# Optimization experiments

Measured on AMD Instinct MI355X. Metric: run time of the kernel, lower is better.

The kernel has to match this reference:

```python
import jax, jax.numpy as jnp
import numpy as np

N, S, E, H = 4, 4096, 1024, 16
D = E // H  # 64


def setup_inputs() -> dict:
    key = jax.random.key(0)
    ks = jax.random.split(key, 6)
    scale = 0.02
    x = jax.random.normal(ks[0], (N, S, E), dtype=jnp.float32)
    Wq = jax.random.normal(ks[1], (E, E), dtype=jnp.float32) * scale
    Wk = jax.random.normal(ks[2], (E, E), dtype=jnp.float32) * scale
    Wv = jax.random.normal(ks[3], (E, E), dtype=jnp.float32) * scale
    Wo = jax.random.normal(ks[4], (E, E), dtype=jnp.float32) * scale
    bo = jax.random.normal(ks[5], (E,), dtype=jnp.float32) * scale
    return {"x": x, "Wq": Wq, "Wk": Wk, "Wv": Wv, "Wo": Wo, "bo": bo}


def reference(x, Wq, Wk, Wv, Wo, bo):
    n, s, _ = x.shape
    # torch nn.Linear(bias=False): y = x @ W.T  (W stored as [out, in])
    q = (x @ Wq.T).reshape(n, s, H, D).transpose(0, 2, 1, 3)  # (N, H, S, D)
    k = (x @ Wk.T).reshape(n, s, H, D).transpose(0, 2, 1, 3)  # (N, H, S, D)
    v = (x @ Wv.T).reshape(n, s, H, D).transpose(0, 2, 1, 3)  # (N, H, S, D)
    # Faithful to source: einsum subscripts applied to the PERMUTED (N,H,S,D)
    # tensors, so label q->H, h->S. energy: (N, H, H, S)
    energy = jnp.einsum('nqhd,nkhd->nqkh', q, k)
    attention = jax.nn.softmax(energy / (D ** 0.5), axis=3)
    # 'nqkh,nvhd->nqhd': k and v are independently summed free indices
    out = jnp.einsum('nqkh,nvhd->nqhd', attention, v).reshape(n, s, E)  # (N,S,E)
    return out @ Wo.T + bo
```

## Files before the change

### kernel.cpp

```cpp
#include <hip/hip_runtime.h>
#include <stdint.h>

typedef unsigned short u16;
typedef unsigned int   u32;
typedef __attribute__((ext_vector_type(8))) short short8;
typedef __attribute__((ext_vector_type(4))) float f32x4;
typedef __attribute__((ext_vector_type(8))) u16   u16x8;

static constexpr size_t NX = (size_t)4 * 4096 * 1024;
static constexpr size_t NW = (size_t)1024 * 1024;

static constexpr size_t OFF_XB   = 0;
static constexpr size_t OFF_EN   = 0;
static constexpr size_t OFF_QK   = 33554432;
static constexpr size_t OFF_WQB  = 100663296;
static constexpr size_t OFF_WKB  = 102760448;
static constexpr size_t OFF_WOB  = 104857600;
static constexpr size_t OFF_WVST = 106954752;
static constexpr size_t OFF_VS   = 107216896;
static constexpr size_t OFF_GMAX = 111411200;
static constexpr size_t OFF_INVZ = 111415296;
static constexpr size_t OFF_A    = 111419392;

static __device__ __forceinline__ u16 f2bf(float f) {
    u32 u = __builtin_bit_cast(u32, f);
    u += 0x7fffu + ((u >> 16) & 1u);
    return (u16)(u >> 16);
}
static __device__ __forceinline__ float bf2f(u16 v) {
    u32 u = ((u32)v) << 16;
    return __builtin_bit_cast(float, u);
}

#if __has_builtin(__builtin_amdgcn_global_load_lds)
#define HAVE_GLOAD_LDS 1
static __device__ __forceinline__ void gload_lds16(const void* g, void* l) {
    __builtin_amdgcn_global_load_lds(
        (__attribute__((address_space(1))) void*)(uintptr_t)g,
        (__attribute__((address_space(3))) void*)(uintptr_t)l,
        16, 0, 0);
}
#endif

#if __has_builtin(__builtin_amdgcn_sched_barrier)
#define SCHED_FENCE() __builtin_amdgcn_sched_barrier(0)
#else
#define SCHED_FENCE()
#endif

__global__ __launch_bounds__(256)
void cvt_kernel(const float* __restrict__ x, const float* __restrict__ wq,
                const float* __restrict__ wk, const float* __restrict__ wo,
                u16* __restrict__ xb, u16* __restrict__ wqb,
                u16* __restrict__ wkb, u16* __restrict__ wob)
{
    size_t i = ((size_t)blockIdx.x * 256 + threadIdx.x) * 8;
    const float* s; u16* dst; size_t o;
    if (i < NX) { s = x; dst = xb; o = i; }
    else {
        size_t r = i - NX;
        int w = (int)(r >> 20);
        o = r & (NW - 1);
        s   = (w == 0) ? wq  : (w == 1) ? wk  : wo;
        dst = (w == 0) ? wqb : (w == 1) ? wkb : wob;
    }
    f32x4 a = *(const f32x4*)&s[o];
    f32x4 c = *(const f32x4*)&s[o + 4];
    u16x8 v;
    v[0]=f2bf(a[0]); v[1]=f2bf(a[1]); v[2]=f2bf(a[2]); v[3]=f2bf(a[3]);
    v[4]=f2bf(c[0]); v[5]=f2bf(c[1]); v[6]=f2bf(c[2]); v[7]=f2bf(c[3]);
    *(u16x8*)&dst[o] = v;
}

__global__ __launch_bounds__(256)
void wvst_kernel(const float* __restrict__ Wv, u16* __restrict__ Bvs)
{
    int idx = blockIdx.x * 256 + threadIdx.x;
    int d = idx >> 10;
    int e = idx & 1023;
    float s = 0.f;
    #pragma unroll
    for (int h = 0; h < 16; ++h) s += Wv[(size_t)(h * 64 + d) * 1024 + e];
    Bvs[(size_t)d * 1024 + e] = f2bf(s);
}

template<bool F32OUT>
__global__ __launch_bounds__(512, 2)
void gemm_bt8(const u16* __restrict__ A, const u16* __restrict__ Bw,
              void* __restrict__ Cv, const float* __restrict__ bias,
              int M, int N, int K, int lognbx)
{
    __shared__ u16 lds[65536];
    const int tid  = threadIdx.x;
    const int wave = tid >> 6;
    const int lane = tid & 63;

    const int nwg = gridDim.x;
    const int swz = ((int)blockIdx.x & 7) * (nwg >> 3) + ((int)blockIdx.x >> 3);
    const long col0 = (long)(swz & ((1 << lognbx) - 1)) * 256;
    const long row0 = (long)(swz >> lognbx) * 256;

    const int wr2 = wave >> 2;
    const int wc2 = wave & 3;
    const int fr  = lane & 15;
    const int kq  = lane >> 4;
    const int rxor = fr & 7;

    const int t255  = tid & 255;
    const int halfA = tid >> 8;
    const int gAsrc = (t255 & 7) ^ ((t255 >> 3) & 7);
    const u16* sA = A + (size_t)(row0 + halfA * 128 + (t255 >> 3)) * K + gAsrc * 8;
    const int dA = halfA * 8192 + t255 * 8;

    const int u  = (tid & 127) | ((tid >> 1) & 128);
    const int bh = (tid >> 7) & 1;
    const int gBsrc = (u & 7) ^ ((u >> 3) & 7);
    const u16* sB = Bw + (size_t)(col0 + bh * 128 + (u >> 3)) * K + gBsrc * 8;
    const int dB = bh * 8192 + u * 8;

    auto STAGE = [&](int buf, int k0) {
        #pragma unroll
        for (int l = 0; l < 4; ++l) {
#ifdef HAVE_GLOAD_LDS
            gload_lds16(sA + (size_t)l * 32 * K + k0, &lds[buf * 16384 + dA + l * 2048]);
            gload_lds16(sB + (size_t)l * 32 * K + k0, &lds[32768 + buf * 16384 + dB + l * 2048]);
#else
            *(short8*)&lds[buf * 16384 + dA + l * 2048] =
                *(const short8*)(sA + (size_t)l * 32 * K + k0);
            *(short8*)&lds[32768 + buf * 16384 + dB + l * 2048] =
                *(const short8*)(sB + (size_t)l * 32 * K + k0);
#endif
        }
    };

    f32x4 acc[8][4] = {};

    STAGE(0, 0);
    __syncthreads();

    const int nt = K >> 6;
    for (int t = 0; t < nt; ++t) {
        const int cur = t & 1;
        const int base  = cur * 16384;
        const int bbase = 32768 + cur * 16384;

        short8 af[4][2], bf[4][2];
        #pragma unroll
        for (int m = 0; m < 4; ++m) {
            const int row = wr2 * 128 + m * 16 + fr;
            #pragma unroll
            for (int kk = 0; kk < 2; ++kk)
                af[m][kk] = *(const short8*)&lds[base + row * 64 + (((kk << 2) | kq) ^ rxor) * 8];
        }
        #pragma unroll
        for (int n = 0; n < 4; ++n) {
            const int col = wc2 * 64 + n * 16 + fr;
            #pragma unroll
            for (int kk = 0; kk < 2; ++kk)
                bf[n][kk] = *(const short8*)&lds[bbase + col * 64 + (((kk << 2) | kq) ^ rxor) * 8];
        }
        if (t + 1 < nt) STAGE(cur ^ 1, (t + 1) << 6);
        SCHED_FENCE();
        __builtin_amdgcn_s_barrier();

        __builtin_amdgcn_s_setprio(1);
        #pragma unroll
        for (int kk = 0; kk < 2; ++kk)
            #pragma unroll
            for (int m = 0; m < 4; ++m)
                #pragma unroll
                for (int n = 0; n < 2; ++n)
                    acc[m][n] = __builtin_amdgcn_mfma_f32_16x16x32_bf16(af[m][kk], bf[n][kk], acc[m][n], 0, 0, 0);
        __builtin_amdgcn_s_setprio(0);
        __builtin_amdgcn_s_barrier();

        __builtin_amdgcn_s_setprio(1);
        #pragma unroll
        for (int kk = 0; kk < 2; ++kk)
            #pragma unroll
            for (int m = 0; m < 4; ++m)
                #pragma unroll
                for (int n = 2; n < 4; ++n)
                    acc[m][n] = __builtin_amdgcn_mfma_f32_16x16x32_bf16(af[m][kk], bf[n][kk], acc[m][n], 0, 0, 0);
        __builtin_amdgcn_s_setprio(0);

        short8 ag[4][2];
        #pragma unroll
        for (int m = 0; m < 4; ++m) {
            const int row = wr2 * 128 + 64 + m * 16 + fr;
            #pragma unroll
            for (int kk = 0; kk < 2; ++kk)
                ag[m][kk] = *(const short8*)&lds[base + row * 64 + (((kk << 2) | kq) ^ rxor) * 8];
        }
        SCHED_FENCE();
        __builtin_amdgcn_s_barrier();

        __builtin_amdgcn_s_setprio(1);
        #pragma unroll
        for (int kk = 0; kk < 2; ++kk)
            #pragma unroll
            for (int m = 0; m < 4; ++m)
                #pragma unroll
                for (int n = 0; n < 2; ++n)
                    acc[m + 4][n] = __builtin_amdgcn_mfma_f32_16x16x32_bf16(ag[m][kk], bf[n][kk], acc[m + 4][n], 0, 0, 0);
        __builtin_amdgcn_s_setprio(0);
        __builtin_amdgcn_s_barrier();

        __builtin_amdgcn_s_setprio(1);
        #pragma unroll
        for (int kk = 0; kk < 2; ++kk)
            #pragma unroll
            for (int m = 0; m < 4; ++m)
                #pragma unroll
                for (int n = 2; n < 4; ++n)
                    acc[m + 4][n] = __builtin_amdgcn_mfma_f32_16x16x32_bf16(ag[m][kk], bf[n][kk], acc[m + 4][n], 0, 0, 0);
        __builtin_amdgcn_s_setprio(0);

        __syncthreads();
    }

    #pragma unroll
    for (int m = 0; m < 8; ++m) {
        #pragma unroll
        for (int n = 0; n < 4; ++n) {
            long gr = row0 + wr2 * 128 + m * 16 + kq * 4;
            long gc = col0 + wc2 * 64 + n * 16 + fr;
            #pragma unroll
            for (int j = 0; j < 4; ++j) {
                float v = acc[m][n][j];
                if (F32OUT) ((float*)Cv)[(gr + j) * N + gc] = v + bias[gc];
                else        ((u16*)  Cv)[(gr + j) * N + gc] = f2bf(v);
            }
        }
    }
}

__global__ __launch_bounds__(256)
void gemm_vs(const u16* __restrict__ A, const u16* __restrict__ Bw,
             float* __restrict__ C)
{
    __shared__ u16 lsA[2][64 * 32];
    __shared__ u16 lsB[2][64 * 32];
    const int tid  = threadIdx.x;
    const int wave = tid >> 6;
    const int lane = tid & 63;
    const long row0 = (long)blockIdx.x * 64;
    const int wr = (wave >> 1) * 32;
    const int wc = (wave & 1) * 32;
    const int fr = lane & 15;
    const int k8 = (lane >> 4) * 8;

    f32x4 acc[2][2] = {};
    const int c0 = tid;
    const u16* pa = &A [(row0 + (c0 >> 2)) * 1024 + (c0 & 3) * 8];
    const u16* pb = &Bw[((size_t)(c0 >> 2)) * 1024 + (c0 & 3) * 8];

    auto STAGE = [&](int buf, int k0) {
#ifdef HAVE_GLOAD_LDS
        gload_lds16(pa + k0, &lsA[buf][wave * 512]);
        gload_lds16(pb + k0, &lsB[buf][wave * 512]);
#else
        *(short8*)&lsA[buf][(size_t)c0 * 8] = *(const short8*)(pa + k0);
        *(short8*)&lsB[buf][(size_t)c0 * 8] = *(const short8*)(pb + k0);
#endif
    };

    STAGE(0, 0);
    __syncthreads();
    for (int t = 0; t < 32; ++t) {
        const int cur = t & 1;
        if (t + 1 < 32) STAGE(cur ^ 1, (t + 1) << 5);
        short8 af[2], bf[2];
        #pragma unroll
        for (int m = 0; m < 2; ++m)
            af[m] = *(const short8*)&lsA[cur][(wr + m * 16 + fr) * 32 + k8];
        #pragma unroll
        for (int n = 0; n < 2; ++n)
            bf[n] = *(const short8*)&lsB[cur][(wc + n * 16 + fr) * 32 + k8];
        #pragma unroll
        for (int m = 0; m < 2; ++m)
            #pragma unroll
            for (int n = 0; n < 2; ++n)
                acc[m][n] = __builtin_amdgcn_mfma_f32_16x16x32_bf16(af[m], bf[n], acc[m][n], 0, 0, 0);
        __syncthreads();
    }

    const int orow = (lane >> 4) * 4;
    #pragma unroll
    for (int m = 0; m < 2; ++m) {
        #pragma unroll
        for (int n = 0; n < 2; ++n) {
            long gr = row0 + wr + m * 16 + orow;
            int  gc = wc + n * 16 + fr;
            #pragma unroll
            for (int j = 0; j < 4; ++j)
                C[(gr + j) * 64 + gc] = acc[m][n][j];
        }
    }
}

__global__ __launch_bounds__(256)
void energy_kernel(const u16* __restrict__ QKb, float* __restrict__ E)
{
    const int lane = threadIdx.x & 63;
    const size_t site = (size_t)blockIdx.x * 4 + (threadIdx.x >> 6);
    const u16* qrow = QKb + site * 2048;
    const int hh = lane & 15;
    const int kg = (lane >> 4) * 8;
    short8 a0 = *(const short8*)&qrow[hh * 64 + kg];
    short8 a1 = *(const short8*)&qrow[hh * 64 + 32 + kg];
    short8 b0 = *(const short8*)&qrow[1024 + hh * 64 + kg];
    short8 b1 = *(const short8*)&qrow[1024 + hh * 64 + 32 + kg];
    f32x4 acc = {};
    acc = __builtin_amdgcn_mfma_f32_16x16x32_bf16(a0, b0, acc, 0, 0, 0);
    acc = __builtin_amdgcn_mfma_f32_16x16x32_bf16(a1, b1, acc, 0, 0, 0);
    float* out = E + site * 256;
    const int ib = (lane >> 4) * 4;
    #pragma unroll
    for (int r = 0; r < 4; ++r)
        out[(ib + r) * 16 + hh] = acc[r];
}

__global__ __launch_bounds__(256)
void stats_part(const float* __restrict__ E, float* __restrict__ pmax,
                float* __restrict__ psum)
{
    const int b = blockIdx.x, p = threadIdx.x;
    const float* e = E + (size_t)b * 64 * 256 + p;
    float m = -3.4e38f;
    float buf[64];
    #pragma unroll 8
    for (int s = 0; s < 64; ++s) {
        float v = e[(size_t)s * 256];
        buf[s] = v;
        m = fmaxf(m, v);
    }
    float z = 0.f;
    #pragma unroll 8
    for (int s = 0; s < 64; ++s) z += __expf((buf[s] - m) * 0.125f);
    pmax[b * 256 + p] = m;
    psum[b * 256 + p] = z;
}
__global__ __launch_bounds__(256)
void stats_comb(const float* __restrict__ pmax, const float* __restrict__ psum,
                float* __restrict__ gmax, float* __restrict__ invZ)
{
    const int n = blockIdx.x, p = threadIdx.x;
    float m = -3.4e38f;
    #pragma unroll 8
    for (int c = 0; c < 64; ++c) m = fmaxf(m, pmax[(n * 64 + c) * 256 + p]);
    float z = 0.f;
    #pragma unroll 8
    for (int c = 0; c < 64; ++c)
        z += psum[(n * 64 + c) * 256 + p] * __expf((pmax[(n * 64 + c) * 256 + p] - m) * 0.125f);
    gmax[n * 256 + p] = m;
    invZ[n * 256 + p] = 1.0f / z;
}

__global__ __launch_bounds__(256)
void a_kernel(const float* __restrict__ E, const float* __restrict__ gmax,
              const float* __restrict__ invZ, float* __restrict__ A)
{
    __shared__ float sm[256], sz[256];
    const int b = blockIdx.x, t = threadIdx.x;
    const int n = b >> 8;
    sm[t] = gmax[n * 256 + t];
    sz[t] = invZ[n * 256 + t];
    __syncthreads();
    const int sl = t >> 4, i = t & 15;
    const size_t srow = (size_t)n * 4096 + (size_t)(b & 255) * 16 + sl;
    const float* e = E + srow * 256 + i * 16;
    float a = 0.f;
    #pragma unroll
    for (int j = 0; j < 16; ++j)
        a += __expf((e[j] - sm[i * 16 + j]) * 0.125f) * sz[i * 16 + j];
    A[srow * 16 + i] = a;
}

__global__ __launch_bounds__(256)
void z2_kernel(const float* __restrict__ A, const float* __restrict__ Vs,
               u16* __restrict__ Z2)
{
    const size_t idx = ((size_t)blockIdx.x * 256 + threadIdx.x) * 8;
    const int e2 = (int)(idx & 1023);
    const size_t row = idx >> 10;
    const int s2 = (int)(row & 4095);
    const int n  = (int)(row >> 12);
    const int i  = s2 >> 8;
    const int s  = ((s2 & 255) << 4) + (e2 >> 6);
    const int d  = e2 & 63;
    const size_t srow = (size_t)n * 4096 + s;
    const float a = A[srow * 16 + i];
    f32x4 v0 = *(const f32x4*)&Vs[srow * 64 + d];
    f32x4 v1 = *(const f32x4*)&Vs[srow * 64 + d + 4];
    u16x8 o;
    o[0]=f2bf(a*v0[0]); o[1]=f2bf(a*v0[1]); o[2]=f2bf(a*v0[2]); o[3]=f2bf(a*v0[3]);
    o[4]=f2bf(a*v1[0]); o[5]=f2bf(a*v1[1]); o[6]=f2bf(a*v1[2]); o[7]=f2bf(a*v1[3]);
    *(u16x8*)&Z2[idx] = o;
}

extern "C" void kernel_launch(void* const* d_in, const int* in_sizes, int n_in,
                              void* d_out, int out_size, void* d_ws, size_t ws_size,
                              hipStream_t stream)
{
    const float* x  = (const float*)d_in[0];
    const float* Wq = (const float*)d_in[1];
    const float* Wk = (const float*)d_in[2];
    const float* Wv = (const float*)d_in[3];
    const float* Wo = (const float*)d_in[4];
    const float* bo = (const float*)d_in[5];
    float* out = (float*)d_out;
    char* ws = (char*)d_ws;

    u16*   xb   = (u16*)  (ws + OFF_XB);
    float* En   = (float*)(ws + OFF_EN);
    u16*   QKb  = (u16*)  (ws + OFF_QK);
    u16*   Z2   = (u16*)  (ws + OFF_QK);
    u16*   Wqb  = (u16*)  (ws + OFF_WQB);
    u16*   Wkb  = (u16*)  (ws + OFF_WKB);
    u16*   Wob  = (u16*)  (ws + OFF_WOB);
    u16*   Bvs  = (u16*)  (ws + OFF_WVST);
    float* Vs   = (float*)(ws + OFF_VS);
    float* gmax = (float*)(ws + OFF_GMAX);
    float* invZ = (float*)(ws + OFF_INVZ);
    float* Ab   = (float*)(ws + OFF_A);
    float* pmax = (float*)(ws + OFF_A);
    float* psum = (float*)(ws + OFF_A + 262144);

    cvt_kernel <<<9728, 256, 0, stream>>>(x, Wq, Wk, Wo, xb, Wqb, Wkb, Wob);
    wvst_kernel<<<256,  256, 0, stream>>>(Wv, Bvs);

    gemm_bt8<false><<<512, 512, 0, stream>>>(xb, Wqb, (void*)QKb, nullptr, 16384, 2048, 1024, 3);
    gemm_vs<<<256, 256, 0, stream>>>(xb, Bvs, Vs);

    energy_kernel<<<4096, 256, 0, stream>>>(QKb, En);

    stats_part<<<256, 256, 0, stream>>>(En, pmax, psum);
    stats_comb<<<4,   256, 0, stream>>>(pmax, psum, gmax, invZ);
    a_kernel  <<<1024, 256, 0, stream>>>(En, gmax, invZ, Ab);
    z2_kernel <<<8192, 256, 0, stream>>>(Ab, Vs, Z2);

    gemm_bt8<true><<<256, 512, 0, stream>>>(Z2, Wob, (void*)out, bo, 16384, 1024, 1024, 2);
}
```

Before: 195.0 us.

## Restructure bf16 GEMM main loop into fine-grained half-tile prefetch pipeline

Rewrites the GEMM K-loop so that A and B tiles are staged in 128-row halves, each issued between MFMA quadrants. Explicit vmcnt/lgkmcnt waits replace full __syncthreads, which lets global-to-LDS loads for tile t+2 overlap compute on tile t. Fragment loads for the next iteration's first quadrant are issued early, and the loop is unrolled by two. The intent is to hide memory latency and cut barrier stalls, at the cost of more barriers per iteration and fragile hand-counted wait counts.

```diff
diff --git a/kernel.cpp b/kernel.cpp
--- a/kernel.cpp
+++ b/kernel.cpp
@@ -47,6 +47,10 @@
 #else
 #define SCHED_FENCE()
 #endif
+#define SBAR() __builtin_amdgcn_s_barrier()
+#define VMCNT6() do { asm volatile("s_waitcnt vmcnt(6)" ::: "memory"); } while (0)
+#define VMCNT0() do { asm volatile("s_waitcnt vmcnt(0)" ::: "memory"); } while (0)
+#define LGKM0()  do { asm volatile("s_waitcnt lgkmcnt(0)" ::: "memory"); } while (0)
 
 __global__ __launch_bounds__(256)
 void cvt_kernel(const float* __restrict__ x, const float* __restrict__ wq,
@@ -96,73 +100,83 @@
     const int lane = tid & 63;
 
     const int nwg = gridDim.x;
-    const int swz = ((int)blockIdx.x & 7) * (nwg >> 3) + ((int)blockIdx.x >> 3);
-    const long col0 = (long)(swz & ((1 << lognbx) - 1)) * 256;
-    const long row0 = (long)(swz >> lognbx) * 256;
+    const int swzb = ((int)blockIdx.x & 7) * (nwg >> 3) + ((int)blockIdx.x >> 3);
+    const long col0 = (long)(swzb & ((1 << lognbx) - 1)) * 256;
+    const long row0 = (long)(swzb >> lognbx) * 256;
 
     const int wr2 = wave >> 2;
     const int wc2 = wave & 3;
     const int fr  = lane & 15;
     const int kq  = lane >> 4;
-    const int rxor = fr & 7;
-
-    const int t255  = tid & 255;
-    const int halfA = tid >> 8;
-    const int gAsrc = (t255 & 7) ^ ((t255 >> 3) & 7);
-    const u16* sA = A + (size_t)(row0 + halfA * 128 + (t255 >> 3)) * K + gAsrc * 8;
-    const int dA = halfA * 8192 + t255 * 8;
-
-    const int u  = (tid & 127) | ((tid >> 1) & 128);
-    const int bh = (tid >> 7) & 1;
-    const int gBsrc = (u & 7) ^ ((u >> 3) & 7);
-    const u16* sB = Bw + (size_t)(col0 + bh * 128 + (u >> 3)) * K + gBsrc * 8;
-    const int dB = bh * 8192 + u * 8;
-
-    auto STAGE = [&](int buf, int k0) {
-        #pragma unroll
-        for (int l = 0; l < 4; ++l) {
+    const int rx  = fr & 7;
+
+    const int G0  = wave * 128 + lane;
+    const int G1  = G0 + 64;
+    const int rr0 = G0 >> 3, g0 = (G0 & 7) ^ (rr0 & 7);
+    const int rr1 = G1 >> 3, g1 = (G1 & 7) ^ (rr1 & 7);
+    const int dst0 = wave * 1024;
+    const int dst1 = wave * 1024 + 512;
+
+    const u16* Abase = A  + row0 * K;
+    const u16* Bbase = Bw + col0 * K;
+
+    auto STAGE_A = [&](int t, int h) {
+        const int slot = ((((t & 1) << 1) | h) << 13);
+        const u16* s = Abase + (size_t)(h * 128) * K + (size_t)(t << 6);
 #ifdef HAVE_GLOAD_LDS
-            gload_lds16(sA + (size_t)l * 32 * K + k0, &lds[buf * 16384 + dA + l * 2048]);
-            gload_lds16(sB + (size_t)l * 32 * K + k0, &lds[32768 + buf * 16384 + dB + l * 2048]);
+        gload_lds16(s + (size_t)rr0 * K + g0 * 8, &lds[slot + dst0]);
+        gload_lds16(s + (size_t)rr1 * K + g1 * 8, &lds[slot + dst1]);
 #else
-            *(short8*)&lds[buf * 16384 + dA + l * 2048] =
-                *(const short8*)(sA + (size_t)l * 32 * K + k0);
-            *(short8*)&lds[32768 + buf * 16384 + dB + l * 2048] =
-                *(const short8*)(sB + (size_t)l * 32 * K + k0);
+        *(short8*)&lds[slot + G0 * 8] = *(const short8*)(s + (size_t)rr0 * K + g0 * 8);
+        *(short8*)&lds[slot + G1 * 8] = *(const short8*)(s + (size_t)rr1 * K + g1 * 8);
 #endif
-        }
     };
+    auto STAGE_B = [&](int t, int h) {
+        const int slot = 32768 + ((((t & 1) << 1) | h) << 13);
+        const u16* s = Bbase + (size_t)(h * 128) * K + (size_t)(t << 6);
+#ifdef HAVE_GLOAD_LDS
+        gload_lds16(s + (size_t)rr0 * K + g0 * 8, &lds[slot + dst0]);
+        gload_lds16(s + (size_t)rr1 * K + g1 * 8, &lds[slot + dst1]);
+#else
+        *(short8*)&lds[slot + G0 * 8] = *(const short8*)(s + (size_t)rr0 * K + g0 * 8);
+        *(short8*)&lds[slot + G1 * 8] = *(const short8*)(s + (size_t)rr1 * K + g1 * 8);
+#endif
+    };
+
+    auto LDA = [&](int t, int m, int kk) -> short8 {
+        const int slot = ((((t & 1) << 1) | wr2) << 13);
+        const int rr = m * 16 + fr;
+        return *(const short8*)&lds[slot + rr * 64 + ((((kk << 2) | kq)) ^ rx) * 8];
+    };
+    auto LDB = [&](int t, int n, int kk) -> short8 {
+        const int slot = 32768 + ((((t & 1) << 1) | (wc2 >> 1)) << 13);
+        const int rr = (wc2 & 1) * 64 + n * 16 + fr;
+        return *(const short8*)&lds[slot + rr * 64 + ((((kk << 2) | kq)) ^ rx) * 8];
+    };
 
     f32x4 acc[8][4] = {};
-
-    STAGE(0, 0);
-    __syncthreads();
+    short8 af0[4][2], af1[4][2], bf0[2][2], bf1[2][2];
+
+    STAGE_A(0, 0); STAGE_A(0, 1); STAGE_B(0, 0); STAGE_B(0, 1);
+    STAGE_A(1, 0); STAGE_A(1, 1); STAGE_B(1, 0);
+    VMCNT6();
+    SCHED_FENCE();
+    SBAR();
+    #pragma unroll
+    for (int m = 0; m < 4; ++m) { af0[m][0] = LDA(0, m, 0); af0[m][1] = LDA(0, m, 1); }
+    #pragma unroll
+    for (int n = 0; n < 2; ++n) { bf0[n][0] = LDB(0, n, 0); bf0[n][1] = LDB(0, n, 1); }
 
     const int nt = K >> 6;
+    #pragma unroll 2
     for (int t = 0; t < nt; ++t) {
-        const int cur = t & 1;
-        const int base  = cur * 16384;
-        const int bbase = 32768 + cur * 16384;
-
-        short8 af[4][2], bf[4][2];
-        #pragma unroll
-        for (int m = 0; m < 4; ++m) {
-            const int row = wr2 * 128 + m * 16 + fr;
-            #pragma unroll
-            for (int kk = 0; kk < 2; ++kk)
-                af[m][kk] = *(const short8*)&lds[base + row * 64 + (((kk << 2) | kq) ^ rxor) * 8];
-        }
-        #pragma unroll
-        for (int n = 0; n < 4; ++n) {
-            const int col = wc2 * 64 + n * 16 + fr;
-            #pragma unroll
-            for (int kk = 0; kk < 2; ++kk)
-                bf[n][kk] = *(const short8*)&lds[bbase + col * 64 + (((kk << 2) | kq) ^ rxor) * 8];
-        }
-        if (t + 1 < nt) STAGE(cur ^ 1, (t + 1) << 6);
+        #pragma unroll
+        for (int n = 0; n < 2; ++n) { bf1[n][0] = LDB(t, n + 2, 0); bf1[n][1] = LDB(t, n + 2, 1); }
+        #pragma unroll
+        for (int m = 0; m < 4; ++m) { af1[m][0] = LDA(t, m + 4, 0); af1[m][1] = LDA(t, m + 4, 1); }
+        if (t + 1 < nt) STAGE_B(t + 1, 1);
         SCHED_FENCE();
-        __builtin_amdgcn_s_barrier();
-
+        SBAR();
         __builtin_amdgcn_s_setprio(1);
         #pragma unroll
         for (int kk = 0; kk < 2; ++kk)
@@ -170,31 +184,14 @@
             for (int m = 0; m < 4; ++m)
                 #pragma unroll
                 for (int n = 0; n < 2; ++n)
-                    acc[m][n] = __builtin_amdgcn_mfma_f32_16x16x32_bf16(af[m][kk], bf[n][kk], acc[m][n], 0, 0, 0);
+                    acc[m][n] = __builtin_amdgcn_mfma_f32_16x16x32_bf16(af0[m][kk], bf0[n][kk], acc[m][n], 0, 0, 0);
         __builtin_amdgcn_s_setprio(0);
-        __builtin_amdgcn_s_barrier();
-
-        __builtin_amdgcn_s_setprio(1);
-        #pragma unroll
-        for (int kk = 0; kk < 2; ++kk)
-            #pragma unroll
-            for (int m = 0; m < 4; ++m)
-                #pragma unroll
-                for (int n = 2; n < 4; ++n)
-                    acc[m][n] = __builtin_amdgcn_mfma_f32_16x16x32_bf16(af[m][kk], bf[n][kk], acc[m][n], 0, 0, 0);
-        __builtin_amdgcn_s_setprio(0);
-
-        short8 ag[4][2];
-        #pragma unroll
-        for (int m = 0; m < 4; ++m) {
-            const int row = wr2 * 128 + 64 + m * 16 + fr;
-            #pragma unroll
-            for (int kk = 0; kk < 2; ++kk)
-                ag[m][kk] = *(const short8*)&lds[base + row * 64 + (((kk << 2) | kq) ^ rxor) * 8];
-        }
+        LGKM0();
         SCHED_FENCE();
-        __builtin_amdgcn_s_barrier();
-
+        SBAR();
+        if (t + 2 < nt) STAGE_A(t + 2, 0);
+        SCHED_FENCE();
+        SBAR();
         __builtin_amdgcn_s_setprio(1);
         #pragma unroll
         for (int kk = 0; kk < 2; ++kk)
@@ -202,21 +199,46 @@
             for (int m = 0; m < 4; ++m)
                 #pragma unroll
                 for (int n = 0; n < 2; ++n)
-                    acc[m + 4][n] = __builtin_amdgcn_mfma_f32_16x16x32_bf16(ag[m][kk], bf[n][kk], acc[m + 4][n], 0, 0, 0);
+                    acc[m][n + 2] = __builtin_amdgcn_mfma_f32_16x16x32_bf16(af0[m][kk], bf1[n][kk], acc[m][n + 2], 0, 0, 0);
         __builtin_amdgcn_s_setprio(0);
-        __builtin_amdgcn_s_barrier();
-
+        SBAR();
+        if (t + 2 < nt) STAGE_A(t + 2, 1);
+        SCHED_FENCE();
+        SBAR();
         __builtin_amdgcn_s_setprio(1);
         #pragma unroll
         for (int kk = 0; kk < 2; ++kk)
             #pragma unroll
             for (int m = 0; m < 4; ++m)
                 #pragma unroll
-                for (int n = 2; n < 4; ++n)
-                    acc[m + 4][n] = __builtin_amdgcn_mfma_f32_16x16x32_bf16(ag[m][kk], bf[n][kk], acc[m + 4][n], 0, 0, 0);
+                for (int n = 0; n < 2; ++n)
+                    acc[m + 4][n] = __builtin_amdgcn_mfma_f32_16x16x32_bf16(af1[m][kk], bf0[n][kk], acc[m + 4][n], 0, 0, 0);
         __builtin_amdgcn_s_setprio(0);
-
-        __syncthreads();
+        SBAR();
+        if (t + 2 < nt) {
+            STAGE_B(t + 2, 0);
+            VMCNT6();
+        } else if (t + 1 < nt) {
+            VMCNT0();
+        }
+        SCHED_FENCE();
+        SBAR();
+        if (t + 1 < nt) {
+            #pragma unroll
+            for (int m = 0; m < 4; ++m) { af0[m][0] = LDA(t + 1, m, 0); af0[m][1] = LDA(t + 1, m, 1); }
+            #pragma unroll
+            for (int n = 0; n < 2; ++n) { bf0[n][0] = LDB(t + 1, n, 0); bf0[n][1] = LDB(t + 1, n, 1); }
+        }
+        __builtin_amdgcn_s_setprio(1);
+        #pragma unroll
+        for (int kk = 0; kk < 2; ++kk)
+            #pragma unroll
+            for (int m = 0; m < 4; ++m)
+                #pragma unroll
+                for (int n = 0; n < 2; ++n)
+                    acc[m + 4][n + 2] = __builtin_amdgcn_mfma_f32_16x16x32_bf16(af1[m][kk], bf1[n][kk], acc[m + 4][n + 2], 0, 0, 0);
+        __builtin_amdgcn_s_setprio(0);
+        SBAR();
     }
 
     #pragma unroll
```

Measured after the change: 202.8 us. 1.04x slower.

## Reassociate output projection via per-slice Vs·Wo products combined with attention weights

Applied to the files above, without the earlier changes.

Replaces materializing the scaled Z2 tensor and the full output GEMM with a small GEMM G = Vs·Wo-slice per head slice. A combine kernel then computes attention weights and mixes 16 G rows per output row with the bias. This removes most of the output-projection FLOPs and the Z2 write/read. In exchange it adds a large fp32 G intermediate in memory. Vs is also stored in bf16 now.

```diff
diff --git a/kernel.cpp b/kernel.cpp
--- a/kernel.cpp
+++ b/kernel.cpp
@@ -20,7 +20,7 @@
 static constexpr size_t OFF_VS   = 107216896;
 static constexpr size_t OFF_GMAX = 111411200;
 static constexpr size_t OFF_INVZ = 111415296;
-static constexpr size_t OFF_A    = 111419392;
+static constexpr size_t OFF_ST   = 111419392;
 
 static __device__ __forceinline__ u16 f2bf(float f) {
     u32 u = __builtin_bit_cast(u32, f);
@@ -84,11 +84,9 @@
     Bvs[(size_t)d * 1024 + e] = f2bf(s);
 }
 
-template<bool F32OUT>
 __global__ __launch_bounds__(512, 2)
-void gemm_bt8(const u16* __restrict__ A, const u16* __restrict__ Bw,
-              void* __restrict__ Cv, const float* __restrict__ bias,
-              int M, int N, int K, int lognbx)
+void gemm_qk(const u16* __restrict__ A, const u16* __restrict__ Bw,
+             u16* __restrict__ C, int M, int N, int K, int lognbx)
 {
     __shared__ u16 lds[65536];
     const int tid  = threadIdx.x;
@@ -226,18 +224,15 @@
             long gr = row0 + wr2 * 128 + m * 16 + kq * 4;
             long gc = col0 + wc2 * 64 + n * 16 + fr;
             #pragma unroll
-            for (int j = 0; j < 4; ++j) {
-                float v = acc[m][n][j];
-                if (F32OUT) ((float*)Cv)[(gr + j) * N + gc] = v + bias[gc];
-                else        ((u16*)  Cv)[(gr + j) * N + gc] = f2bf(v);
-            }
+            for (int j = 0; j < 4; ++j)
+                C[(gr + j) * N + gc] = f2bf(acc[m][n][j]);
         }
     }
 }
 
 __global__ __launch_bounds__(256)
 void gemm_vs(const u16* __restrict__ A, const u16* __restrict__ Bw,
-             float* __restrict__ C)
+             u16* __restrict__ C)
 {
     __shared__ u16 lsA[2][64 * 32];
     __shared__ u16 lsB[2][64 * 32];
@@ -294,7 +289,7 @@
             int  gc = wc + n * 16 + fr;
             #pragma unroll
             for (int j = 0; j < 4; ++j)
-                C[(gr + j) * 64 + gc] = acc[m][n][j];
+                C[(gr + j) * 64 + gc] = f2bf(acc[m][n][j]);
         }
     }
 }
@@ -358,45 +353,113 @@
 }
 
 __global__ __launch_bounds__(256)
-void a_kernel(const float* __restrict__ E, const float* __restrict__ gmax,
-              const float* __restrict__ invZ, float* __restrict__ A)
-{
-    __shared__ float sm[256], sz[256];
-    const int b = blockIdx.x, t = threadIdx.x;
-    const int n = b >> 8;
+void g_kernel(const u16* __restrict__ Vsb, const u16* __restrict__ Wob,
+              float* __restrict__ G)
+{
+    __shared__ u16 lA[64 * 64];
+    __shared__ u16 lB[256 * 64];
+    const int tid = threadIdx.x;
+    const int wave = tid >> 6, lane = tid & 63;
+    const int op = blockIdx.x, uc = blockIdx.y, sl = blockIdx.z;
+
+    {
+        const int j = tid >> 2;
+        const size_t srow = (size_t)16 * (64 * uc + j) + sl;
+        #pragma unroll
+        for (int h = 0; h < 2; ++h) {
+            const int g = (tid & 3) + h * 4;
+            u16x8 v = *(const u16x8*)&Vsb[srow * 64 + g * 8];
+            *(u16x8*)&lA[j * 64 + ((g ^ (j & 7)) * 8)] = v;
+        }
+    }
+    {
+        const size_t o = (size_t)op * 256 + tid;
+        #pragma unroll
+        for (int g = 0; g < 8; ++g) {
+            u16x8 v = *(const u16x8*)&Wob[o * 1024 + 64 * sl + g * 8];
+            *(u16x8*)&lB[tid * 64 + ((g ^ (tid & 7)) * 8)] = v;
+        }
+    }
+    __syncthreads();
+
+    const int fr = lane & 15, kq = lane >> 4;
+    f32x4 acc[4][4] = {};
+    #pragma unroll
+    for (int kk = 0; kk < 2; ++kk) {
+        short8 af[4], bq[4];
+        #pragma unroll
+        for (int m = 0; m < 4; ++m) {
+            const int j = m * 16 + fr;
+            af[m] = *(const short8*)&lA[j * 64 + (((kq + 4 * kk) ^ (j & 7)) * 8)];
+        }
+        #pragma unroll
+        for (int n = 0; n < 4; ++n) {
+            const int o = wave * 64 + n * 16 + fr;
+            bq[n] = *(const short8*)&lB[o * 64 + (((kq + 4 * kk) ^ (o & 7)) * 8)];
+        }
+        #pragma unroll
+        for (int m = 0; m < 4; ++m)
+            #pragma unroll
+            for (int n = 0; n < 4; ++n)
+                acc[m][n] = __builtin_amdgcn_mfma_f32_16x16x32_bf16(af[m], bq[n], acc[m][n], 0, 0, 0);
+    }
+
+    #pragma unroll
+    for (int m = 0; m < 4; ++m) {
+        #pragma unroll
+        for (int n = 0; n < 4; ++n) {
+            const int ocol = op * 256 + wave * 64 + n * 16 + fr;
+            #pragma unroll
+            for (int jj = 0; jj < 4; ++jj) {
+                const int j = m * 16 + kq * 4 + jj;
+                G[((size_t)16 * (64 * uc + j) + sl) * 1024 + ocol] = acc[m][n][jj];
+            }
+        }
+    }
+}
+
+__global__ __launch_bounds__(256)
+void comb_kernel(const float* __restrict__ En, const float* __restrict__ gmax,
+                 const float* __restrict__ invZ, const float* __restrict__ G,
+                 const float* __restrict__ bo, float* __restrict__ out)
+{
+    __shared__ float sm[256], sz[256], sa[256];
+    const int b = blockIdx.x;
+    const int n = b >> 8, c = b & 255;
+    const int t = threadIdx.x;
     sm[t] = gmax[n * 256 + t];
     sz[t] = invZ[n * 256 + t];
     __syncthreads();
-    const int sl = t >> 4, i = t & 15;
-    const size_t srow = (size_t)n * 4096 + (size_t)(b & 255) * 16 + sl;
-    const float* e = E + srow * 256 + i * 16;
-    float a = 0.f;
-    #pragma unroll
-    for (int j = 0; j < 16; ++j)
-        a += __expf((e[j] - sm[i * 16 + j]) * 0.125f) * sz[i * 16 + j];
-    A[srow * 16 + i] = a;
-}
-
-__global__ __launch_bounds__(256)
-void z2_kernel(const float* __restrict__ A, const float* __restrict__ Vs,
-               u16* __restrict__ Z2)
-{
-    const size_t idx = ((size_t)blockIdx.x * 256 + threadIdx.x) * 8;
-    const int e2 = (int)(idx & 1023);
-    const size_t row = idx >> 10;
-    const int s2 = (int)(row & 4095);
-    const int n  = (int)(row >> 12);
-    const int i  = s2 >> 8;
-    const int s  = ((s2 & 255) << 4) + (e2 >> 6);
-    const int d  = e2 & 63;
-    const size_t srow = (size_t)n * 4096 + s;
-    const float a = A[srow * 16 + i];
-    f32x4 v0 = *(const f32x4*)&Vs[srow * 64 + d];
-    f32x4 v1 = *(const f32x4*)&Vs[srow * 64 + d + 4];
-    u16x8 o;
-    o[0]=f2bf(a*v0[0]); o[1]=f2bf(a*v0[1]); o[2]=f2bf(a*v0[2]); o[3]=f2bf(a*v0[3]);
-    o[4]=f2bf(a*v1[0]); o[5]=f2bf(a*v1[1]); o[6]=f2bf(a*v1[2]); o[7]=f2bf(a*v1[3]);
-    *(u16x8*)&Z2[idx] = o;
+    {
+        const int sl = t >> 4, i = t & 15;
+        const float* e = En + ((size_t)n * 4096 + c * 16 + sl) * 256 + i * 16;
+        float a = 0.f;
+        #pragma unroll
+        for (int j = 0; j < 16; ++j)
+            a += __expf((e[j] - sm[i * 16 + j]) * 0.125f) * sz[i * 16 + j];
+        sa[sl * 16 + i] = a;
+    }
+    __syncthreads();
+
+    const int o0 = t * 4;
+    const float* gp = G + ((size_t)n * 4096 + c * 16) * 1024 + o0;
+    f32x4 g[16];
+    #pragma unroll
+    for (int sl = 0; sl < 16; ++sl) g[sl] = *(const f32x4*)&gp[(size_t)sl * 1024];
+    const f32x4 b4 = *(const f32x4*)&bo[o0];
+    #pragma unroll
+    for (int i = 0; i < 16; ++i) {
+        f32x4 acc = b4;
+        #pragma unroll
+        for (int sl = 0; sl < 16; ++sl) {
+            const float a = sa[sl * 16 + i];
+            acc[0] += a * g[sl][0];
+            acc[1] += a * g[sl][1];
+            acc[2] += a * g[sl][2];
+            acc[3] += a * g[sl][3];
+        }
+        *(f32x4*)&out[((size_t)n * 4096 + i * 256 + c) * 1024 + o0] = acc;
+    }
 }
 
 extern "C" void kernel_launch(void* const* d_in, const int* in_sizes, int n_in,
@@ -415,30 +478,29 @@
     u16*   xb   = (u16*)  (ws + OFF_XB);
     float* En   = (float*)(ws + OFF_EN);
     u16*   QKb  = (u16*)  (ws + OFF_QK);
-    u16*   Z2   = (u16*)  (ws + OFF_QK);
+    float* G    = (float*)(ws + OFF_QK);
     u16*   Wqb  = (u16*)  (ws + OFF_WQB);
     u16*   Wkb  = (u16*)  (ws + OFF_WKB);
     u16*   Wob  = (u16*)  (ws + OFF_WOB);
     u16*   Bvs  = (u16*)  (ws + OFF_WVST);
-    float* Vs   = (float*)(ws + OFF_VS);
+    u16*   Vsb  = (u16*)  (ws + OFF_VS);
     float* gmax = (float*)(ws + OFF_GMAX);
     float* invZ = (float*)(ws + OFF_INVZ);
-    float* Ab   = (float*)(ws + OFF_A);
-    float* pmax = (float*)(ws + OFF_A);
-    float* psum = (float*)(ws + OFF_A + 262144);
+    float* pmax = (float*)(ws + OFF_ST);
+    float* psum = (float*)(ws + OFF_ST + 262144);
 
     cvt_kernel <<<9728, 256, 0, stream>>>(x, Wq, Wk, Wo, xb, Wqb, Wkb, Wob);
     wvst_kernel<<<256,  256, 0, stream>>>(Wv, Bvs);
 
-    gemm_bt8<false><<<512, 512, 0, stream>>>(xb, Wqb, (void*)QKb, nullptr, 16384, 2048, 1024, 3);
-    gemm_vs<<<256, 256, 0, stream>>>(xb, Bvs, Vs);
+    gemm_qk<<<512, 512, 0, stream>>>(xb, Wqb, QKb, 16384, 2048, 1024, 3);
+    gemm_vs<<<256, 256, 0, stream>>>(xb, Bvs, Vsb);
 
     energy_kernel<<<4096, 256, 0, stream>>>(QKb, En);
 
     stats_part<<<256, 256, 0, stream>>>(En, pmax, psum);
     stats_comb<<<4,   256, 0, stream>>>(pmax, psum, gmax, invZ);
-    a_kernel  <<<1024, 256, 0, stream>>>(En, gmax, invZ, Ab);
-    z2_kernel <<<8192, 256, 0, stream>>>(Ab, Vs, Z2);
-
-    gemm_bt8<true><<<256, 512, 0, stream>>>(Z2, Wob, (void*)out, bo, 16384, 1024, 1024, 2);
-}
+
+    g_kernel<<<dim3(4, 16, 16), 256, 0, stream>>>(Vsb, Wob, G);
+
+    comb_kernel<<<1024, 256, 0, stream>>>(En, gmax, invZ, G, bo, out);
+}
```

Result: faster. 185.3 us (-5.0%).
